# Performance work log

Measured on AMD Instinct MI355X. Metric: run time of the kernel, lower is better.

Reference implementation:

```python
import jax, jax.numpy as jnp
import numpy as np

NUM_HEADS = 16
KEY_DIM = 64
VALUE_DIM = 64
D_MODEL = 1024
NEG_INF = -1e10


def setup_inputs() -> dict:
    key = jax.random.key(0)
    ks = jax.random.split(key, 8)
    B, T, S, D = 4, 2048, 2048, D_MODEL
    w_scale = 1.0 / np.sqrt(D)  # keep logits well-scaled
    inp = {
        'query': jax.random.normal(ks[0], (B, T, D), jnp.float32),
        'key':   jax.random.normal(ks[1], (B, S, D), jnp.float32),
        'value': jax.random.normal(ks[2], (B, S, D), jnp.float32),
        'Wq': jax.random.normal(ks[3], (D, NUM_HEADS * KEY_DIM), jnp.float32) * w_scale,
        'bq': jnp.zeros((NUM_HEADS * KEY_DIM,), jnp.float32),
        'Wk': jax.random.normal(ks[4], (D, NUM_HEADS * KEY_DIM), jnp.float32) * w_scale,
        'bk': jnp.zeros((NUM_HEADS * KEY_DIM,), jnp.float32),
        'Wv': jax.random.normal(ks[5], (D, NUM_HEADS * VALUE_DIM), jnp.float32) * w_scale,
        'bv': jnp.zeros((NUM_HEADS * VALUE_DIM,), jnp.float32),
        'Wo': jax.random.normal(ks[6], (NUM_HEADS * VALUE_DIM, D), jnp.float32) * w_scale,
        'bo': jnp.zeros((D,), jnp.float32),
    }
    return inp


def reference(query, key, value, Wq, bq, Wk, bk, Wv, bv, Wo, bo):
    B, T, _ = query.shape
    S = key.shape[1]
    H, Dk, Dv = NUM_HEADS, KEY_DIM, VALUE_DIM
    # QKV projections -> (B, T/S, H, D_head)
    q = (query @ Wq + bq).reshape(B, T, H, Dk)
    k = (key @ Wk + bk).reshape(B, S, H, Dk)
    v = (value @ Wv + bv).reshape(B, S, H, Dv)
    # scaled dot-product scores: (B, H, T, S)
    q = q * (1.0 / jnp.sqrt(jnp.asarray(Dk, q.dtype)))
    scores = jnp.einsum('bthd,bshd->bhts', q, k)
    # causal mask [1,1,T,S], additive -1e10 on masked positions (as in source)
    causal = jnp.tril(jnp.ones((T, S), scores.dtype))
    scores = scores + NEG_INF * (1.0 - causal)
    attn = jax.nn.softmax(scores, axis=-1)
    # dropout rate = 0.0 -> identity
    ctx = jnp.einsum('bhts,bshd->bthd', attn, v).reshape(B, T, H * Dv)
    out = ctx @ Wo + bo
    return out
```

## Files before the change

### kernel.cpp

```cpp
#include <hip/hip_runtime.h>
#include <cstdint>

#define DEV static __device__ __forceinline__

typedef unsigned short u16;
typedef unsigned int u32;
using short8 = __attribute__((ext_vector_type(8))) short;
using f32x4  = __attribute__((ext_vector_type(4))) float;
using f32x16 = __attribute__((ext_vector_type(16))) float;
using u32x4  = __attribute__((ext_vector_type(4))) unsigned int;

constexpr int Bz = 4, Tz = 2048, Dz = 1024, Hz = 16;
constexpr float QSCALE = 0.125f * 1.4426950408889634f;

DEV u16 f2bf(float x) {
  union { float f; u32 u; } c; c.f = x;
  u32 u = c.u;
  return (u16)((u + 0x7FFFu + ((u >> 16) & 1u)) >> 16);
}

DEV u32 cvtpk(float a, float b) {
  u32 r;
  asm("v_cvt_pk_bf16_f32 %0, %1, %2" : "=v"(r) : "v"(a), "v"(b));
  return r;
}

DEV void gload16(const void* g, void* l) {
  __builtin_amdgcn_global_load_lds(
      (const __attribute__((address_space(1))) void*)g,
      (__attribute__((address_space(3))) void*)l, 16, 0, 0);
}

__global__ void wt_kernel(const float* __restrict__ W0, const float* __restrict__ W1,
                          const float* __restrict__ W2, const float* __restrict__ W3,
                          u16* __restrict__ T0, u16* __restrict__ T1,
                          u16* __restrict__ T2, u16* __restrict__ T3) {
  __shared__ float tile[32][33];
  int z = blockIdx.z;
  const float* W = z == 0 ? W0 : z == 1 ? W1 : z == 2 ? W2 : W3;
  u16* WT = z == 0 ? T0 : z == 1 ? T1 : z == 2 ? T2 : T3;
  int n0 = blockIdx.x * 32, k0 = blockIdx.y * 32;
  int tx = threadIdx.x & 31, ty = threadIdx.x >> 5;
  #pragma unroll
  for (int i = 0; i < 32; i += 8)
    tile[ty + i][tx] = W[(size_t)(k0 + ty + i) * Dz + n0 + tx];
  __syncthreads();
  #pragma unroll
  for (int i = 0; i < 32; i += 8)
    WT[(size_t)(n0 + ty + i) * Dz + k0 + tx] = f2bf(tile[tx][ty + i]);
}

__global__ __launch_bounds__(256) void vt_kernel(const u16* __restrict__ V,
                                                 u16* __restrict__ VT) {
  __shared__ char t[8192];
  int bh = blockIdx.y, tt0 = blockIdx.x * 64;
  int tid = threadIdx.x;
  const char* src = (const char*)(V + ((size_t)bh * Tz + tt0) * 64);
  #pragma unroll
  for (int i = 0; i < 2; ++i) {
    int c = tid + i * 256;
    int row = c >> 3, colb = (c & 7) * 16;
    *(uint4*)(t + row * 128 + (colb ^ ((row & 7) << 4))) =
        *(const uint4*)(src + (size_t)row * 128 + colb);
  }
  __syncthreads();
  int dv = tid >> 2, ts = (tid & 3) * 16;
  u32 w[8];
  #pragma unroll
  for (int p = 0; p < 8; ++p) {
    int t1 = ts + 2 * p, t2 = t1 + 1;
    u32 lo = *(const u16*)(t + t1 * 128 + ((dv * 2) ^ ((t1 & 7) << 4)));
    u32 hi = *(const u16*)(t + t2 * 128 + ((dv * 2) ^ ((t2 & 7) << 4)));
    w[p] = lo | (hi << 16);
  }
  u16* dst = VT + ((size_t)bh * 64 + dv) * Tz + tt0 + ts;
  *(uint4*)(dst)     = uint4{w[0], w[1], w[2], w[3]};
  *(uint4*)(dst + 8) = uint4{w[4], w[5], w[6], w[7]};
}

template <int AMODE, int EPI>
DEV void gemm_core(const void* __restrict__ Aptr, const u16* __restrict__ WT,
                   const float* __restrict__ bias, void* __restrict__ Cptr,
                   float scale, int n0, int m0, char* ldsraw)
{
  char* L = ldsraw;

  const int tid = threadIdx.x;
  const int lane = tid & 63, wid = tid >> 6;
  const int g = lane >> 4, l15 = lane & 15;
  const int wm = (wid >> 1) * 64, wn = (wid & 1) * 64;

  f32x4 acc[4][4] = {};
  float4 areg[8];

  auto loadA = [&](int k0) {
    const float* A = (const float*)Aptr;
    #pragma unroll
    for (int i = 0; i < 8; ++i) {
      int c = tid + i * 256;
      int row = c >> 4, f0 = (c & 15) * 4;
      areg[i] = *(const float4*)(A + (size_t)(m0 + row) * Dz + k0 + f0);
    }
  };
  auto writeA = [&](int buf) {
    char* Lb = L + buf * 32768;
    #pragma unroll
    for (int i = 0; i < 8; ++i) {
      int c = tid + i * 256;
      int row = c >> 4, f0 = (c & 15) * 4;
      uint2 p = make_uint2(cvtpk(areg[i].x, areg[i].y), cvtpk(areg[i].z, areg[i].w));
      *(uint2*)(Lb + row * 128 + ((f0 * 2) ^ ((row & 7) << 4))) = p;
    }
  };
  auto stageA16 = [&](int buf, int k0) {
    const u16* A = (const u16*)Aptr;
    char* Lb = L + buf * 32768;
    #pragma unroll
    for (int i = 0; i < 4; ++i) {
      int c = tid + i * 256;
      int row = c >> 3, colb = (c & 7) * 16;
      int cbs = colb ^ ((row & 7) << 4);
      gload16(A + (size_t)(m0 + row) * Dz + k0 + (cbs >> 1), Lb + c * 16);
    }
  };
  auto stageB = [&](int buf, int k0) {
    char* Lb = L + buf * 32768 + 16384;
    #pragma unroll
    for (int i = 0; i < 4; ++i) {
      int c = tid + i * 256;
      int row = c >> 3, colb = (c & 7) * 16;
      int cbs = colb ^ ((row & 7) << 4);
      gload16(WT + (size_t)(n0 + row) * Dz + k0 + (cbs >> 1), Lb + c * 16);
    }
  };

  if (AMODE == 0) { loadA(0); stageB(0, 0); writeA(0); }
  else            { stageA16(0, 0); stageB(0, 0); }
  __syncthreads();

  int cur = 0;
  for (int step = 0; step < 16; ++step) {
    if (step < 15) {
      if (AMODE == 0) loadA((step + 1) * 64);
      else            stageA16(cur ^ 1, (step + 1) * 64);
      stageB(cur ^ 1, (step + 1) * 64);
    }
    const char* Ab = L + cur * 32768;
    const char* Bb = Ab + 16384;
    #pragma unroll
    for (int kc = 0; kc < 2; ++kc) {
      short8 af[4], bfv[4];
      #pragma unroll
      for (int mt = 0; mt < 4; ++mt) {
        int row = wm + mt * 16 + l15;
        af[mt] = *(const short8*)(Ab + row * 128 + ((kc * 64 + g * 16) ^ ((row & 7) << 4)));
      }
      #pragma unroll
      for (int nt = 0; nt < 4; ++nt) {
        int row = wn + nt * 16 + l15;
        bfv[nt] = *(const short8*)(Bb + row * 128 + ((kc * 64 + g * 16) ^ ((row & 7) << 4)));
      }
      #pragma unroll
      for (int mt = 0; mt < 4; ++mt)
        #pragma unroll
        for (int nt = 0; nt < 4; ++nt)
          acc[mt][nt] = __builtin_amdgcn_mfma_f32_16x16x32_bf16(af[mt], bfv[nt], acc[mt][nt], 0, 0, 0);
    }
    if (AMODE == 0 && step < 15) writeA(cur ^ 1);
    __syncthreads();
    cur ^= 1;
  }

  if (EPI == 0) {
    u16* C = (u16*)Cptr;
    #pragma unroll
    for (int nt = 0; nt < 4; ++nt) {
      int n = n0 + wn + nt * 16 + l15;
      float bv = bias[n];
      int h = n >> 6, dh = n & 63;
      #pragma unroll
      for (int mt = 0; mt < 4; ++mt)
        #pragma unroll
        for (int r = 0; r < 4; ++r) {
          int m = m0 + wm + mt * 16 + g * 4 + r;
          int bb = m >> 11, t = m & 2047;
          float val = (acc[mt][nt][r] + bv) * scale;
          C[((size_t)(bb * Hz + h) * Tz + t) * 64 + dh] = f2bf(val);
        }
    }
  } else {
    float* C = (float*)Cptr;
    #pragma unroll
    for (int nt = 0; nt < 4; ++nt) {
      int n = n0 + wn + nt * 16 + l15;
      float bv = bias[n];
      #pragma unroll
      for (int mt = 0; mt < 4; ++mt)
        #pragma unroll
        for (int r = 0; r < 4; ++r) {
          int m = m0 + wm + mt * 16 + g * 4 + r;
          C[(size_t)m * Dz + n] = acc[mt][nt][r] + bv;
        }
    }
  }
}

__global__ __launch_bounds__(256) void qkv_kernel(
    const float* __restrict__ Aq, const float* __restrict__ Ak, const float* __restrict__ Av,
    const u16* __restrict__ Wq, const u16* __restrict__ Wk, const u16* __restrict__ Wv,
    const float* __restrict__ bq, const float* __restrict__ bk, const float* __restrict__ bv,
    u16* __restrict__ oq, u16* __restrict__ ok, u16* __restrict__ ov)
{
  __shared__ char lds[65536];
  int z = blockIdx.z;
  const float* A = z == 0 ? Aq : z == 1 ? Ak : Av;
  const u16* W   = z == 0 ? Wq : z == 1 ? Wk : Wv;
  const float* b = z == 0 ? bq : z == 1 ? bk : bv;
  u16* C         = z == 0 ? oq : z == 1 ? ok : ov;
  float scale    = z == 0 ? QSCALE : 1.0f;
  gemm_core<0, 0>(A, W, b, C, scale, blockIdx.y * 128, blockIdx.x * 128, lds);
}

__global__ __launch_bounds__(256) void out_gemm_kernel(
    const u16* __restrict__ A, const u16* __restrict__ WT,
    const float* __restrict__ bias, float* __restrict__ C)
{
  __shared__ char lds[65536];
  gemm_core<1, 1>(A, WT, bias, C, 1.0f, blockIdx.y * 128, blockIdx.x * 128, lds);
}

DEV short8 mk_pb(float p0, float p1, float p2, float p3,
                 float p4, float p5, float p6, float p7) {
  u32 x0 = cvtpk(p0, p1), y0 = cvtpk(p4, p5);
  u32 x1 = cvtpk(p2, p3), y1 = cvtpk(p6, p7);
  asm("v_permlane32_swap_b32 %0, %1" : "+v"(x0), "+v"(y0));
  asm("v_permlane32_swap_b32 %0, %1" : "+v"(x1), "+v"(y1));
  u32x4 w = {x0, x1, y0, y1};
  return __builtin_bit_cast(short8, w);
}

__global__ __launch_bounds__(512) void attn_kernel(
    const u16* __restrict__ Q, const u16* __restrict__ K,
    const u16* __restrict__ VT, u16* __restrict__ CTX)
{
  __shared__ char lds[65536];

  const int tid = threadIdx.x;
  const int lane = tid & 63, wave = tid >> 6;
  const int s = wave >> 2, w4 = wave & 3;
  const int l31 = lane & 31, hi = lane >> 5;
  const int pr = blockIdx.x;
  const int bh = blockIdx.y;
  const int b = bh >> 4, h = bh & 15;

  const u16* qb  = Q  + (size_t)bh * Tz * 64;
  const u16* kb  = K  + (size_t)bh * Tz * 64;
  const u16* vtb = VT + (size_t)bh * 64 * Tz;

  #pragma unroll 1
  for (int half = 0; half < 2; ++half) {
    const int j = half ? (15 - pr) : pr;
    const int t0 = j * 128;
    const int nsteps = j + 1;
    const int wq0 = t0 + w4 * 32;
    const int qg = wq0 + l31, wqhi = wq0 + 31;
    const int tbase = s * nsteps;

    auto stage = [&](int buf, int step) {
      #pragma unroll
      for (int i = 0; i < 4; ++i) {
        int c = tid + i * 512;
        int sc = c >> 10, r = c & 1023;
        int tn = r >> 9, e = r & 511;
        int row = e >> 3, colb = (e & 7) * 16;
        int cbs = colb ^ ((row & 7) << 4);
        int kv0 = (sc * nsteps + step) * 64;
        char* dst = lds + ((sc * 2 + buf) << 14) + (tn << 13) + e * 16;
        if (tn == 0)
          gload16(kb + (size_t)(kv0 + row) * 64 + (cbs >> 1), dst);
        else
          gload16(vtb + (size_t)row * Tz + kv0 + (cbs >> 1), dst);
      }
    };

    stage(0, 0);

    short8 qf[4];
    #pragma unroll
    for (int kc = 0; kc < 4; ++kc)
      qf[kc] = *(const short8*)(qb + (size_t)qg * 64 + kc * 16 + hi * 8);

    f32x16 o0 = {}, o1 = {};
    float m_run = -3.0e38f, l_run = 0.f;

    __syncthreads();

    int cur = 0;
    for (int step = 0; step < nsteps; ++step) {
      if (step + 1 < nsteps) stage(cur ^ 1, step + 1);
      const int kv0 = (tbase + step) * 64;

      if (kv0 <= wqhi) {
        const char* Kl = lds + ((s * 2 + cur) << 14);
        const char* Vl = Kl + 8192;
        const int swz = (l31 & 7) << 4;

        f32x16 s0 = {}, s1 = {};
        #pragma unroll
        for (int kc = 0; kc < 4; ++kc) {
          int cb = (kc * 32 + hi * 16) ^ swz;
          short8 kf0 = *(const short8*)(Kl + l31 * 128 + cb);
          short8 kf1 = *(const short8*)(Kl + (32 + l31) * 128 + cb);
          s0 = __builtin_amdgcn_mfma_f32_32x32x16_bf16(kf0, qf[kc], s0, 0, 0, 0);
          s1 = __builtin_amdgcn_mfma_f32_32x32x16_bf16(kf1, qf[kc], s1, 0, 0, 0);
        }

        if (kv0 + 63 > wq0) {
          #pragma unroll
          for (int r = 0; r < 16; ++r) {
            int kg = kv0 + (r & 3) + 8 * (r >> 2) + 4 * hi;
            if (kg > qg)      s0[r] = -3.0e38f;
            if (kg + 32 > qg) s1[r] = -3.0e38f;
          }
        }

        float tmax = fmaxf(s0[0], s1[0]);
        #pragma unroll
        for (int r = 1; r < 16; ++r) tmax = fmaxf(tmax, fmaxf(s0[r], s1[r]));
        tmax = fmaxf(tmax, __shfl_xor(tmax, 32));

        if (__any(tmax > m_run + 8.f)) {
          float m_new = fmaxf(m_run, tmax);
          float sc = __builtin_amdgcn_exp2f(m_run - m_new);
          l_run *= sc;
          #pragma unroll
          for (int r = 0; r < 16; ++r) { o0[r] *= sc; o1[r] *= sc; }
          m_run = m_new;
        }
        float psum = 0.f;
        #pragma unroll
        for (int r = 0; r < 16; ++r) {
          s0[r] = __builtin_amdgcn_exp2f(s0[r] - m_run); psum += s0[r];
          s1[r] = __builtin_amdgcn_exp2f(s1[r] - m_run); psum += s1[r];
        }
        psum += __shfl_xor(psum, 32);
        l_run += psum;

        short8 pb0 = mk_pb(s0[0], s0[1], s0[2],  s0[3],  s0[4],  s0[5],  s0[6],  s0[7]);
        short8 pb1 = mk_pb(s0[8], s0[9], s0[10], s0[11], s0[12], s0[13], s0[14], s0[15]);
        short8 pb2 = mk_pb(s1[0], s1[1], s1[2],  s1[3],  s1[4],  s1[5],  s1[6],  s1[7]);
        short8 pb3 = mk_pb(s1[8], s1[9], s1[10], s1[11], s1[12], s1[13], s1[14], s1[15]);

        #pragma unroll
        for (int kc = 0; kc < 4; ++kc) {
          int cb = (kc * 32 + hi * 16) ^ swz;
          short8 vf0 = *(const short8*)(Vl + l31 * 128 + cb);
          short8 vf1 = *(const short8*)(Vl + (32 + l31) * 128 + cb);
          short8 pbk = (kc == 0) ? pb0 : (kc == 1) ? pb1 : (kc == 2) ? pb2 : pb3;
          o0 = __builtin_amdgcn_mfma_f32_32x32x16_bf16(vf0, pbk, o0, 0, 0, 0);
          o1 = __builtin_amdgcn_mfma_f32_32x32x16_bf16(vf1, pbk, o1, 0, 0, 0);
        }
      }

      __syncthreads();
      cur ^= 1;
    }

    if (s == 1) {
      char* P = lds + w4 * 9216 + lane * 144;
      #pragma unroll
      for (int r2 = 0; r2 < 4; ++r2) {
        f32x4 a = {o0[4*r2], o0[4*r2+1], o0[4*r2+2], o0[4*r2+3]};
        *(f32x4*)(P + r2 * 16) = a;
        f32x4 c = {o1[4*r2], o1[4*r2+1], o1[4*r2+2], o1[4*r2+3]};
        *(f32x4*)(P + 64 + r2 * 16) = c;
      }
      *(float*)(P + 128) = m_run;
      *(float*)(P + 132) = l_run;
    }
    __syncthreads();
    if (s == 0) {
      const char* P = lds + w4 * 9216 + lane * 144;
      float m1 = *(const float*)(P + 128), l1 = *(const float*)(P + 132);
      float m = fmaxf(m_run, m1);
      float w0 = __builtin_amdgcn_exp2f(m_run - m);
      float w1 = __builtin_amdgcn_exp2f(m1 - m);
      float inv = 1.0f / (w0 * l_run + w1 * l1);

      u16* cp = CTX + ((size_t)(b * Tz + qg)) * Dz + h * 64;
      #pragma unroll
      for (int rq = 0; rq < 4; ++rq) {
        f32x4 p0 = *(const f32x4*)(P + rq * 16);
        f32x4 p1 = *(const f32x4*)(P + 64 + rq * 16);
        int dv0 = 8 * rq + 4 * hi;
        float a0 = (w0 * o0[rq*4+0] + w1 * p0[0]) * inv;
        float a1 = (w0 * o0[rq*4+1] + w1 * p0[1]) * inv;
        float a2 = (w0 * o0[rq*4+2] + w1 * p0[2]) * inv;
        float a3 = (w0 * o0[rq*4+3] + w1 * p0[3]) * inv;
        *(uint2*)(cp + dv0) = make_uint2(cvtpk(a0, a1), cvtpk(a2, a3));
        float c0 = (w0 * o1[rq*4+0] + w1 * p1[0]) * inv;
        float c1 = (w0 * o1[rq*4+1] + w1 * p1[1]) * inv;
        float c2 = (w0 * o1[rq*4+2] + w1 * p1[2]) * inv;
        float c3 = (w0 * o1[rq*4+3] + w1 * p1[3]) * inv;
        *(uint2*)(cp + 32 + dv0) = make_uint2(cvtpk(c0, c1), cvtpk(c2, c3));
      }
    }
    __syncthreads();
  }
}

extern "C" void kernel_launch(void* const* d_in, const int* in_sizes, int n_in,
                              void* d_out, int out_size, void* d_ws, size_t ws_size,
                              hipStream_t stream) {
  (void)in_sizes; (void)n_in; (void)out_size; (void)ws_size;
  const float* query = (const float*)d_in[0];
  const float* key   = (const float*)d_in[1];
  const float* value = (const float*)d_in[2];
  const float* Wq = (const float*)d_in[3];
  const float* bq = (const float*)d_in[4];
  const float* Wk = (const float*)d_in[5];
  const float* bk = (const float*)d_in[6];
  const float* Wv = (const float*)d_in[7];
  const float* bv = (const float*)d_in[8];
  const float* Wo = (const float*)d_in[9];
  const float* bo = (const float*)d_in[10];

  char* ws = (char*)d_ws;
  const size_t SZ_ACT = (size_t)Bz * Tz * Dz * sizeof(u16);
  const size_t SZ_W = (size_t)Dz * Dz * sizeof(u16);
  u16* qw  = (u16*)(ws);
  u16* kw  = (u16*)(ws + SZ_ACT);
  u16* vw  = (u16*)(ws + 2 * SZ_ACT);
  u16* vtw = (u16*)(ws + 3 * SZ_ACT);
  u16* cw  = vw;
  u16* wqt = (u16*)(ws + 4 * SZ_ACT);
  u16* wkt = (u16*)(ws + 4 * SZ_ACT + SZ_W);
  u16* wvt = (u16*)(ws + 4 * SZ_ACT + 2 * SZ_W);
  u16* wot = (u16*)(ws + 4 * SZ_ACT + 3 * SZ_W);

  wt_kernel<<<dim3(32, 32, 4), 256, 0, stream>>>(Wq, Wk, Wv, Wo, wqt, wkt, wvt, wot);

  qkv_kernel<<<dim3(64, 8, 3), 256, 0, stream>>>(query, key, value,
                                                 wqt, wkt, wvt,
                                                 bq, bk, bv,
                                                 qw, kw, vw);

  vt_kernel<<<dim3(Tz / 64, Bz * Hz), 256, 0, stream>>>(vw, vtw);

  attn_kernel<<<dim3(8, Bz * Hz), 512, 0, stream>>>(qw, kw, vtw, cw);

  out_gemm_kernel<<<dim3(64, 8), 256, 0, stream>>>(cw, wot, bo, (float*)d_out);
}
```

Baseline: 201.2 us.

## Single-buffer GEMM LDS for higher occupancy and store QKV in row-major layout

The QKV projection now writes Q/K/V in plain (B,T,H*D) row-major order instead of a head-major scatter, and the attention and V-transpose kernels read with a stride of Dz. The shared GEMM core goes from double-buffered LDS (64KB) to a single 32KB buffer with two barriers per k-step, and declares launch_bounds(256,4) so more blocks can reside per CU. The fp32 A-load indexing is also reorganised. The aim is to trade explicit software pipelining for occupancy-based latency hiding and coalesced epilogue stores, at the risk of exposing load latency within each block.

```diff
diff --git a/kernel.cpp b/kernel.cpp
--- a/kernel.cpp
+++ b/kernel.cpp
@@ -54,14 +54,15 @@
                                                  u16* __restrict__ VT) {
   __shared__ char t[8192];
   int bh = blockIdx.y, tt0 = blockIdx.x * 64;
+  int b = bh >> 4, h = bh & 15;
   int tid = threadIdx.x;
-  const char* src = (const char*)(V + ((size_t)bh * Tz + tt0) * 64);
+  const char* src = (const char*)(V + ((size_t)(b * Tz + tt0)) * Dz + h * 64);
   #pragma unroll
   for (int i = 0; i < 2; ++i) {
     int c = tid + i * 256;
     int row = c >> 3, colb = (c & 7) * 16;
     *(uint4*)(t + row * 128 + (colb ^ ((row & 7) << 4))) =
-        *(const uint4*)(src + (size_t)row * 128 + colb);
+        *(const uint4*)(src + (size_t)row * (Dz * 2) + colb);
   }
   __syncthreads();
   int dv = tid >> 2, ts = (tid & 3) * 16;
@@ -81,10 +82,8 @@
 template <int AMODE, int EPI>
 DEV void gemm_core(const void* __restrict__ Aptr, const u16* __restrict__ WT,
                    const float* __restrict__ bias, void* __restrict__ Cptr,
-                   float scale, int n0, int m0, char* ldsraw)
+                   float scale, int n0, int m0, char* L)
 {
-  char* L = ldsraw;
-
   const int tid = threadIdx.x;
   const int lane = tid & 63, wid = tid >> 6;
   const int g = lane >> 4, l15 = lane & 15;
@@ -93,72 +92,65 @@
   f32x4 acc[4][4] = {};
   float4 areg[8];
 
+  const float* Af = (const float*)Aptr;
+
   auto loadA = [&](int k0) {
-    const float* A = (const float*)Aptr;
     #pragma unroll
     for (int i = 0; i < 8; ++i) {
-      int c = tid + i * 256;
-      int row = c >> 4, f0 = (c & 15) * 4;
-      areg[i] = *(const float4*)(A + (size_t)(m0 + row) * Dz + k0 + f0);
+      int row = (tid >> 4) + i * 16, f0 = (tid & 15) * 4;
+      areg[i] = *(const float4*)(Af + (size_t)(m0 + row) * Dz + k0 + f0);
     }
   };
-  auto writeA = [&](int buf) {
-    char* Lb = L + buf * 32768;
+  auto writeA = [&]() {
     #pragma unroll
     for (int i = 0; i < 8; ++i) {
-      int c = tid + i * 256;
-      int row = c >> 4, f0 = (c & 15) * 4;
+      int row = (tid >> 4) + i * 16, f0 = (tid & 15) * 4;
       uint2 p = make_uint2(cvtpk(areg[i].x, areg[i].y), cvtpk(areg[i].z, areg[i].w));
-      *(uint2*)(Lb + row * 128 + ((f0 * 2) ^ ((row & 7) << 4))) = p;
+      *(uint2*)(L + row * 128 + ((f0 * 2) ^ ((row & 7) << 4))) = p;
     }
   };
-  auto stageA16 = [&](int buf, int k0) {
+  auto stageA16 = [&](int k0) {
     const u16* A = (const u16*)Aptr;
-    char* Lb = L + buf * 32768;
     #pragma unroll
     for (int i = 0; i < 4; ++i) {
       int c = tid + i * 256;
       int row = c >> 3, colb = (c & 7) * 16;
       int cbs = colb ^ ((row & 7) << 4);
-      gload16(A + (size_t)(m0 + row) * Dz + k0 + (cbs >> 1), Lb + c * 16);
+      gload16(A + (size_t)(m0 + row) * Dz + k0 + (cbs >> 1), L + c * 16);
     }
   };
-  auto stageB = [&](int buf, int k0) {
-    char* Lb = L + buf * 32768 + 16384;
+  auto stageB = [&](int k0) {
     #pragma unroll
     for (int i = 0; i < 4; ++i) {
       int c = tid + i * 256;
       int row = c >> 3, colb = (c & 7) * 16;
       int cbs = colb ^ ((row & 7) << 4);
-      gload16(WT + (size_t)(n0 + row) * Dz + k0 + (cbs >> 1), Lb + c * 16);
+      gload16(WT + (size_t)(n0 + row) * Dz + k0 + (cbs >> 1), L + 16384 + c * 16);
     }
   };
 
-  if (AMODE == 0) { loadA(0); stageB(0, 0); writeA(0); }
-  else            { stageA16(0, 0); stageB(0, 0); }
-  __syncthreads();
-
-  int cur = 0;
+  if (AMODE == 0) loadA(0);
+
   for (int step = 0; step < 16; ++step) {
-    if (step < 15) {
-      if (AMODE == 0) loadA((step + 1) * 64);
-      else            stageA16(cur ^ 1, (step + 1) * 64);
-      stageB(cur ^ 1, (step + 1) * 64);
-    }
-    const char* Ab = L + cur * 32768;
-    const char* Bb = Ab + 16384;
+    const int k0 = step * 64;
+    stageB(k0);
+    if (AMODE == 0) writeA();
+    else            stageA16(k0);
+    __syncthreads();
+    if (AMODE == 0 && step < 15) loadA(k0 + 64);
+
     #pragma unroll
     for (int kc = 0; kc < 2; ++kc) {
       short8 af[4], bfv[4];
       #pragma unroll
       for (int mt = 0; mt < 4; ++mt) {
         int row = wm + mt * 16 + l15;
-        af[mt] = *(const short8*)(Ab + row * 128 + ((kc * 64 + g * 16) ^ ((row & 7) << 4)));
+        af[mt] = *(const short8*)(L + row * 128 + ((kc * 64 + g * 16) ^ ((row & 7) << 4)));
       }
       #pragma unroll
       for (int nt = 0; nt < 4; ++nt) {
         int row = wn + nt * 16 + l15;
-        bfv[nt] = *(const short8*)(Bb + row * 128 + ((kc * 64 + g * 16) ^ ((row & 7) << 4)));
+        bfv[nt] = *(const short8*)(L + 16384 + row * 128 + ((kc * 64 + g * 16) ^ ((row & 7) << 4)));
       }
       #pragma unroll
       for (int mt = 0; mt < 4; ++mt)
@@ -166,9 +158,7 @@
         for (int nt = 0; nt < 4; ++nt)
           acc[mt][nt] = __builtin_amdgcn_mfma_f32_16x16x32_bf16(af[mt], bfv[nt], acc[mt][nt], 0, 0, 0);
     }
-    if (AMODE == 0 && step < 15) writeA(cur ^ 1);
     __syncthreads();
-    cur ^= 1;
   }
 
   if (EPI == 0) {
@@ -177,15 +167,12 @@
     for (int nt = 0; nt < 4; ++nt) {
       int n = n0 + wn + nt * 16 + l15;
       float bv = bias[n];
-      int h = n >> 6, dh = n & 63;
       #pragma unroll
       for (int mt = 0; mt < 4; ++mt)
         #pragma unroll
         for (int r = 0; r < 4; ++r) {
           int m = m0 + wm + mt * 16 + g * 4 + r;
-          int bb = m >> 11, t = m & 2047;
-          float val = (acc[mt][nt][r] + bv) * scale;
-          C[((size_t)(bb * Hz + h) * Tz + t) * 64 + dh] = f2bf(val);
+          C[(size_t)m * Dz + n] = f2bf((acc[mt][nt][r] + bv) * scale);
         }
     }
   } else {
@@ -205,13 +192,13 @@
   }
 }
 
-__global__ __launch_bounds__(256) void qkv_kernel(
+__global__ __launch_bounds__(256, 4) void qkv_kernel(
     const float* __restrict__ Aq, const float* __restrict__ Ak, const float* __restrict__ Av,
     const u16* __restrict__ Wq, const u16* __restrict__ Wk, const u16* __restrict__ Wv,
     const float* __restrict__ bq, const float* __restrict__ bk, const float* __restrict__ bv,
     u16* __restrict__ oq, u16* __restrict__ ok, u16* __restrict__ ov)
 {
-  __shared__ char lds[65536];
+  __shared__ char lds[32768];
   int z = blockIdx.z;
   const float* A = z == 0 ? Aq : z == 1 ? Ak : Av;
   const u16* W   = z == 0 ? Wq : z == 1 ? Wk : Wv;
@@ -221,11 +208,11 @@
   gemm_core<0, 0>(A, W, b, C, scale, blockIdx.y * 128, blockIdx.x * 128, lds);
 }
 
-__global__ __launch_bounds__(256) void out_gemm_kernel(
+__global__ __launch_bounds__(256, 4) void out_gemm_kernel(
     const u16* __restrict__ A, const u16* __restrict__ WT,
     const float* __restrict__ bias, float* __restrict__ C)
 {
-  __shared__ char lds[65536];
+  __shared__ char lds[32768];
   gemm_core<1, 1>(A, WT, bias, C, 1.0f, blockIdx.y * 128, blockIdx.x * 128, lds);
 }
 
@@ -253,8 +240,8 @@
   const int bh = blockIdx.y;
   const int b = bh >> 4, h = bh & 15;
 
-  const u16* qb  = Q  + (size_t)bh * Tz * 64;
-  const u16* kb  = K  + (size_t)bh * Tz * 64;
+  const u16* qb  = Q  + (size_t)b * Tz * Dz + h * 64;
+  const u16* kb  = K  + (size_t)b * Tz * Dz + h * 64;
   const u16* vtb = VT + (size_t)bh * 64 * Tz;
 
   #pragma unroll 1
@@ -277,7 +264,7 @@
         int kv0 = (sc * nsteps + step) * 64;
         char* dst = lds + ((sc * 2 + buf) << 14) + (tn << 13) + e * 16;
         if (tn == 0)
-          gload16(kb + (size_t)(kv0 + row) * 64 + (cbs >> 1), dst);
+          gload16(kb + (size_t)(kv0 + row) * Dz + (cbs >> 1), dst);
         else
           gload16(vtb + (size_t)row * Tz + kv0 + (cbs >> 1), dst);
       }
@@ -288,7 +275,7 @@
     short8 qf[4];
     #pragma unroll
     for (int kc = 0; kc < 4; ++kc)
-      qf[kc] = *(const short8*)(qb + (size_t)qg * 64 + kc * 16 + hi * 8);
+      qf[kc] = *(const short8*)(qb + (size_t)qg * Dz + kc * 16 + hi * 8);
 
     f32x16 o0 = {}, o1 = {};
     float m_run = -3.0e38f, l_run = 0.f;
```

Result: slower. 209.3 us (+4.1%).
